# Performance work log

Hardware: AMD Instinct MI355X
Metric: run time of the kernel (lower is better)

## Reference

```python
import jax, jax.numpy as jnp
import numpy as np
import math

DIM, NH, HD = 4096, 32, 128
B, S = 2, 2048
MAX_SEQ, INIT_SLICE = 4096, 2048  # init_slice = max_seq_len - max_prompt_size
NEG = -1e9


def setup_inputs() -> dict:
    key = jax.random.key(0)
    ks = jax.random.split(key, 6)
    x = jax.random.normal(ks[0], (B, S, DIM), dtype=jnp.float32)
    scale = 1.0 / math.sqrt(DIM)
    wq = jax.random.normal(ks[1], (DIM, DIM), dtype=jnp.float32) * scale
    wk = jax.random.normal(ks[2], (DIM, DIM), dtype=jnp.float32) * scale
    wv = jax.random.normal(ks[3], (DIM, DIM), dtype=jnp.float32) * scale
    wo = jax.random.normal(ks[4], (DIM, DIM), dtype=jnp.float32) * scale
    # RoPE frequencies, viewed as real pairs [S, HD//2, 2] = (cos, sin)
    inv_freq = 1.0 / (10000.0 ** (jnp.arange(0, HD, 2, dtype=jnp.float32) / HD))
    ang = jnp.arange(S, dtype=jnp.float32)[:, None] * inv_freq[None, :]  # [S, HD//2]
    freqs_cis_real = jnp.stack([jnp.cos(ang), jnp.sin(ang)], axis=-1)
    # causal additive mask [1,1,S,S]
    mask = jnp.where(jnp.triu(jnp.ones((S, S), dtype=bool), k=1), NEG, 0.0)[None, None].astype(jnp.float32)
    cache_k = jnp.zeros((B, MAX_SEQ, NH, HD), dtype=jnp.float32)
    cache_v = jnp.zeros((B, MAX_SEQ, NH, HD), dtype=jnp.float32)
    return {"x": x, "freqs_cis_real": freqs_cis_real, "mask": mask,
            "wq": wq, "wk": wk, "wv": wv, "wo": wo,
            "cache_k": cache_k, "cache_v": cache_v, "slice_size": 2048}


def _apply_rotary(xq, xk, freqs_cis_real):
    # xq, xk: [b, s, h, d]; pairs along last dim are (real, imag)
    b, s, h, d = xq.shape
    fr = freqs_cis_real[None, :, None, :, 0]  # [1, s, 1, d//2]
    fi = freqs_cis_real[None, :, None, :, 1]

    def rot(t):
        t = t.reshape(b, s, h, d // 2, 2)
        tr, ti = t[..., 0], t[..., 1]
        out = jnp.stack([tr * fr - ti * fi, tr * fi + ti * fr], axis=-1)
        return out.reshape(b, s, h, d)

    return rot(xq), rot(xk)


def reference(x, freqs_cis_real, mask, wq, wk, wv, wo, cache_k, cache_v, slice_size):
    bsz, seqlen, _ = x.shape
    xq = (x @ wq.T).reshape(bsz, seqlen, NH, HD)
    xk = (x @ wk.T).reshape(bsz, seqlen, NH, HD)
    xv = (x @ wv.T).reshape(bsz, seqlen, NH, HD)
    xq, xk = _apply_rotary(xq, xk, freqs_cis_real)
    # prompt-phase (seqlen > 1) cache update: cat(cache[:, :init_slice], new)
    cache_k_new = jnp.concatenate([cache_k[:bsz, :INIT_SLICE], xk], axis=1)
    cache_v_new = jnp.concatenate([cache_v[:bsz, :INIT_SLICE], xv], axis=1)
    keys = cache_k_new[:, -slice_size:]    # [b, k, h, d]
    values = cache_v_new[:, -slice_size:]
    scores = jnp.einsum('bqhd,bkhd->bhqk', xq, keys) / math.sqrt(HD)
    scores = scores + mask
    probs = jax.nn.softmax(scores.astype(jnp.float32), axis=-1).astype(xq.dtype)
    out = jnp.einsum('bhqk,bkhd->bqhd', probs, values).reshape(bsz, seqlen, -1)
    return out @ wo.T
```

## Files before the change

### kernel.cpp

```cpp
#include <hip/hip_runtime.h>
#include <hip/hip_bf16.h>
#include <stdint.h>

#define SEQ   2048
#define NHEAD 32
#define HDIM  128
#define DMODEL 4096
#define MTOT  4096
#define RSCALE 0.08838834764831845f

typedef __hip_bfloat16 bf16_t;
typedef __attribute__((ext_vector_type(8))) short short8v;
typedef __attribute__((ext_vector_type(4))) short short4v;
typedef __attribute__((ext_vector_type(4))) float f32x4;

typedef __attribute__((address_space(3))) void lds_void;
typedef __attribute__((address_space(1))) void gbl_void;
#define TO_LDS(p) ((lds_void*)(uint32_t)(uintptr_t)(p))
#define TO_GBL(p) ((gbl_void*)(uintptr_t)(p))
#define ASYNC_CP16(g, l) __builtin_amdgcn_global_load_lds(TO_GBL(g), TO_LDS(l), 16, 0, 0)

__device__ __forceinline__ float bf2f(short u) {
  union { uint32_t i; float f; } x; x.i = ((uint32_t)(uint16_t)u) << 16; return x.f;
}

__global__ __launch_bounds__(256) void cast_f32_to_bf16(const float* __restrict__ in,
                                                        bf16_t* __restrict__ out) {
  size_t i = (size_t)blockIdx.x * 256 + threadIdx.x;
  const f32x4* p = (const f32x4*)in + i * 2;
  f32x4 a = p[0], b = p[1];
  __align__(16) bf16_t tmp[8];
#pragma unroll
  for (int j = 0; j < 4; ++j) tmp[j]     = __float2bfloat16(a[j]);
#pragma unroll
  for (int j = 0; j < 4; ++j) tmp[4 + j] = __float2bfloat16(b[j]);
  *(short8v*)(out + i * 8) = *(const short8v*)tmp;
}

#define GEMM_SUBITER(J, VMC, DO_ISSUE)                                         \
  {                                                                            \
    asm volatile("s_waitcnt vmcnt(" #VMC ")" ::: "memory");                    \
    __builtin_amdgcn_s_barrier();                                              \
    __builtin_amdgcn_sched_barrier(0);                                         \
    const char* sl = (const char*)&lds[(J) & 3][0];                            \
    short8v a[8], b[4];                                                        \
    _Pragma("unroll")                                                          \
    for (int m = 0; m < 8; ++m)                                                \
      a[m] = *(const short8v*)(sl + aoff + m * 1024);                          \
    _Pragma("unroll")                                                          \
    for (int n = 0; n < 4; ++n)                                                \
      b[n] = *(const short8v*)(sl + boff + n * 1024);                          \
    if (DO_ISSUE) {                                                            \
      const int jn = (J) + 3;                                                  \
      char* dl = (char*)&lds[jn & 3][0] + stoff;                               \
      const bf16_t* ga = gA + (size_t)jn * 32;                                 \
      const bf16_t* gb = gB + (size_t)jn * 32;                                 \
      ASYNC_CP16(ga,              dl);                                         \
      ASYNC_CP16(ga + 128 * 4096, dl + 8192);                                  \
      ASYNC_CP16(gb,              dl + 16384);                                 \
      ASYNC_CP16(gb + 128 * 4096, dl + 24576);                                 \
    }                                                                          \
    __builtin_amdgcn_s_setprio(1);                                             \
    _Pragma("unroll")                                                          \
    for (int m = 0; m < 8; ++m)                                                \
      _Pragma("unroll")                                                        \
      for (int n = 0; n < 4; ++n)                                              \
        acc[m][n] = __builtin_amdgcn_mfma_f32_16x16x32_bf16(a[m], b[n],        \
                                                            acc[m][n], 0, 0, 0); \
    __builtin_amdgcn_s_setprio(0);                                             \
  }

template <bool OUT_BF16>
__global__ __launch_bounds__(512, 2) void gemm_nt(const bf16_t* __restrict__ A,
                                                  const bf16_t* __restrict__ B0,
                                                  const bf16_t* __restrict__ B1,
                                                  const bf16_t* __restrict__ B2,
                                                  void* __restrict__ Cout) {
  __shared__ bf16_t lds[4][16384];
  const int z = blockIdx.z;
  const bf16_t* __restrict__ Bm = (z == 0) ? B0 : (z == 1 ? B1 : B2);
  const int tid = threadIdx.x;
  const int wave = tid >> 6, lane = tid & 63;
  const int bid = blockIdx.x;
  const int xcd = bid & 7, idx = bid >> 3;
  const int bm = (xcd >> 1) * 4 + (idx >> 3);
  const int bn = (xcd & 1) * 8 + (idx & 7);
  const int wr = wave >> 2, wc = wave & 3;
  const int r = lane & 15, g = lane >> 4;

  f32x4 acc[8][4] = {};

  const int srow = wave * 16 + (lane >> 2);
  const int scol = (lane & 3) * 8;
  const bf16_t* gA = A  + ((size_t)bm * 256 + srow) * 4096 + scol;
  const bf16_t* gB = Bm + ((size_t)bn * 256 + srow) * 4096 + scol;
  const int stoff = wave * 1024 + lane * 16;

  const int aoff = (wr * 128 + r) * 64 + g * 16;
  const int boff = 16384 + (wc * 64 + r) * 64 + g * 16;

#pragma unroll
  for (int j0 = 0; j0 < 3; ++j0) {
    char* dl = (char*)&lds[j0][0] + stoff;
    const bf16_t* ga = gA + (size_t)j0 * 32;
    const bf16_t* gb = gB + (size_t)j0 * 32;
    ASYNC_CP16(ga,              dl);
    ASYNC_CP16(ga + 128 * 4096, dl + 8192);
    ASYNC_CP16(gb,              dl + 16384);
    ASYNC_CP16(gb + 128 * 4096, dl + 24576);
  }

  for (int j = 0; j < 125; ++j) GEMM_SUBITER(j, 8, true);
  GEMM_SUBITER(125, 8, false);
  GEMM_SUBITER(126, 4, false);
  GEMM_SUBITER(127, 0, false);

  const size_t row_base = (size_t)bm * 256 + wr * 128 + g * 4;
  const size_t col_base = (size_t)bn * 256 + wc * 64 + r;
  if (OUT_BF16) {
    bf16_t* C = (bf16_t*)Cout + (size_t)z * 16777216u;
#pragma unroll
    for (int m = 0; m < 8; ++m)
#pragma unroll
      for (int n = 0; n < 4; ++n)
#pragma unroll
        for (int j = 0; j < 4; ++j)
          C[(row_base + m * 16 + j) * 4096 + col_base + n * 16] = __float2bfloat16(acc[m][n][j]);
  } else {
    float* C = (float*)Cout;
#pragma unroll
    for (int m = 0; m < 8; ++m)
#pragma unroll
      for (int n = 0; n < 4; ++n)
#pragma unroll
        for (int j = 0; j < 4; ++j)
          C[(row_base + m * 16 + j) * 4096 + col_base + n * 16] = acc[m][n][j];
  }
}

__global__ __launch_bounds__(256) void rope_kernel(const bf16_t* __restrict__ qkv,
                                                   const float* __restrict__ freqs,
                                                   bf16_t* __restrict__ qrot,
                                                   bf16_t* __restrict__ krot) {
  const int which = blockIdx.y;
  const bf16_t* __restrict__ src = qkv + (size_t)which * 16777216u;
  bf16_t* __restrict__ dst = (which == 0) ? qrot : krot;
  const float sc = (which == 0) ? RSCALE : 1.0f;
  size_t t = (size_t)blockIdx.x * 256 + threadIdx.x;
  int dg = t & 15;
  int s  = (int)(t >> 4) & 2047;
  int bh = (int)(t >> 15);
  int b  = bh >> 5;
  int d0 = dg * 8;

  short8v v = *(const short8v*)&src[((size_t)(b * 2048 + s)) * 4096 + (bh & 31) * 128 + d0];
  const float* fp = freqs + (size_t)s * 128 + d0;
  f32x4 f0 = *(const f32x4*)fp;
  f32x4 f1 = *(const f32x4*)(fp + 4);
  float fr[4] = {f0[0], f0[2], f1[0], f1[2]};
  float fi[4] = {f0[1], f0[3], f1[1], f1[3]};
  __align__(16) bf16_t tmp[8];
#pragma unroll
  for (int i = 0; i < 4; ++i) {
    float tr = bf2f(v[2 * i]), ti = bf2f(v[2 * i + 1]);
    tmp[2 * i]     = __float2bfloat16((tr * fr[i] - ti * fi[i]) * sc);
    tmp[2 * i + 1] = __float2bfloat16((tr * fi[i] + ti * fr[i]) * sc);
  }
  *(short8v*)&dst[((size_t)bh * 2048 + s) * 128 + d0] = *(const short8v*)tmp;
}

__global__ __launch_bounds__(256) void vtrans_kernel(const bf16_t* __restrict__ xv,
                                                     bf16_t* __restrict__ vt) {
  __shared__ bf16_t tile[64 * 136];
  const int s0 = blockIdx.x * 64;
  const int bh = blockIdx.y;
  const int b = bh >> 5, h = bh & 31;
  const int tid = threadIdx.x;
#pragma unroll
  for (int it = 0; it < 4; ++it) {
    int c = it * 256 + tid;
    int row = c >> 4, col8 = c & 15;
    short8v v = *(const short8v*)&xv[((size_t)(b * 2048 + s0 + row)) * 4096 + h * 128 + col8 * 8];
    *(short8v*)&tile[row * 136 + col8 * 8] = v;
  }
  __syncthreads();
#pragma unroll
  for (int it = 0; it < 4; ++it) {
    int c = it * 256 + tid;
    int d = c >> 3, sc = c & 7;
    __align__(16) bf16_t tmp[8];
#pragma unroll
    for (int i = 0; i < 8; ++i) tmp[i] = tile[(sc * 8 + i) * 136 + d];
    *(short8v*)&vt[((size_t)(bh * 128 + d)) * 2048 + s0 + sc * 8] = *(const short8v*)tmp;
  }
}

#define PSTR 72
__global__ __launch_bounds__(512) void attn_kernel(const bf16_t* __restrict__ qrot,
                                                   const bf16_t* __restrict__ krot,
                                                   const bf16_t* __restrict__ vt,
                                                   bf16_t* __restrict__ att) {
  __shared__ bf16_t Kls[64 * 128];
  __shared__ bf16_t Vls[128 * 64];
  __shared__ bf16_t Pls[8][16 * PSTR];

  const int lid  = blockIdx.x;
  const int xcd  = lid & 7;
  const int kk_  = lid >> 3;
  const int bh   = xcd + 8 * ((kk_ >> 4) & 7);
  const int qidx = 15 - (kk_ & 15);
  const int warp = threadIdx.x >> 6;
  const int lane = threadIdx.x & 63;
  const int r = lane & 15, g = lane >> 4;

  const bf16_t* __restrict__ Q  = qrot + (size_t)bh * 2048 * 128;
  const bf16_t* __restrict__ Kp = krot + (size_t)bh * 2048 * 128;
  const bf16_t* __restrict__ Vt = vt   + (size_t)bh * 128 * 2048;
  bf16_t* __restrict__ Pw = &Pls[warp][0];

  const int qB = qidx * 128 + warp * 16;
  const int ntiles = 2 * qidx + 2;

  short8v qf[4];
#pragma unroll
  for (int kk = 0; kk < 4; ++kk)
    qf[kk] = *(const short8v*)&Q[(size_t)(qB + r) * 128 + kk * 32 + g * 8];

  float l = 0.f;
  f32x4 o[8];
#pragma unroll
  for (int n2 = 0; n2 < 8; ++n2) o[n2] = f32x4{0.f, 0.f, 0.f, 0.f};

  const int rA = lane >> 4, cA = lane & 15;
  const int rB = lane >> 3, cB = lane & 7;
  const int swz = (r & 7) << 4;

  for (int t = 0; t < ntiles; ++t) {
    const int kb = t * 64;

#pragma unroll
    for (int i = 0; i < 2; ++i) {
      const int krow = warp * 8 + i * 4 + rA;
      const int kcol = 8 * (cA ^ ((i * 4 + rA) & 7));
      ASYNC_CP16(Kp + (size_t)(kb + krow) * 128 + kcol,
                 (char*)Kls + (size_t)(krow * 128 + cA * 8) * 2);
    }
#pragma unroll
    for (int i = 0; i < 2; ++i) {
      const int vrow = warp * 16 + i * 8 + rB;
      const int vcol = 8 * (cB ^ rB);
      ASYNC_CP16(Vt + (size_t)vrow * 2048 + kb + vcol,
                 (char*)Vls + (size_t)(vrow * 64 + cB * 8) * 2);
    }
    __syncthreads();

    if (kb <= qB + 15) {
      f32x4 sacc[4];
#pragma unroll
      for (int n = 0; n < 4; ++n) sacc[n] = f32x4{0.f, 0.f, 0.f, 0.f};
#pragma unroll
      for (int n = 0; n < 4; ++n)
#pragma unroll
        for (int kk = 0; kk < 4; ++kk) {
          short8v kf = *(const short8v*)((const char*)Kls +
                         (n * 16 + r) * 256 + ((kk * 64 + g * 16) ^ swz));
          sacc[n] = __builtin_amdgcn_mfma_f32_16x16x32_bf16(kf, qf[kk], sacc[n], 0, 0, 0);
        }

      float p[16];
#pragma unroll
      for (int n = 0; n < 4; ++n)
#pragma unroll
        for (int j = 0; j < 4; ++j)
          p[n * 4 + j] = __expf(sacc[n][j]);

      if (kb + 63 > qB) {
        const int qa = qB + r;
#pragma unroll
        for (int n = 0; n < 4; ++n)
#pragma unroll
          for (int j = 0; j < 4; ++j)
            if (kb + n * 16 + g * 4 + j > qa) p[n * 4 + j] = 0.f;
      }

      {
        float ts[8];
#pragma unroll
        for (int i = 0; i < 8; ++i) ts[i] = p[i] + p[i + 8];
#pragma unroll
        for (int i = 0; i < 4; ++i) ts[i] += ts[i + 4];
        float rs = (ts[0] + ts[1]) + (ts[2] + ts[3]);
        rs += __shfl_xor(rs, 16, 64);
        rs += __shfl_xor(rs, 32, 64);
        l += rs;
      }

#pragma unroll
      for (int n = 0; n < 4; ++n) {
        __align__(8) bf16_t tp[4];
#pragma unroll
        for (int j = 0; j < 4; ++j) tp[j] = __float2bfloat16(p[n * 4 + j]);
        *(short4v*)&Pw[r * PSTR + n * 16 + g * 4] = *(const short4v*)tp;
      }

#pragma unroll
      for (int kk2 = 0; kk2 < 2; ++kk2) {
        short8v pf = *(const short8v*)&Pw[r * PSTR + kk2 * 32 + g * 8];
#pragma unroll
        for (int n2 = 0; n2 < 8; ++n2) {
          short8v vf = *(const short8v*)((const char*)Vls +
                         (n2 * 16 + r) * 128 + ((kk2 * 64 + g * 16) ^ swz));
          o[n2] = __builtin_amdgcn_mfma_f32_16x16x32_bf16(pf, vf, o[n2], 0, 0, 0);
        }
      }
    }
    __syncthreads();
  }

  float lq[4];
#pragma unroll
  for (int j = 0; j < 4; ++j) lq[j] = 1.0f / __shfl(l, g * 4 + j, 64);
  const int b = bh >> 5, h = bh & 31;
#pragma unroll
  for (int n2 = 0; n2 < 8; ++n2)
#pragma unroll
    for (int j = 0; j < 4; ++j)
      att[((size_t)(b * 2048 + qB + g * 4 + j)) * 4096 + h * 128 + n2 * 16 + r] =
          __float2bfloat16(o[n2][j] * lq[j]);
}

extern "C" void kernel_launch(void* const* d_in, const int* in_sizes, int n_in,
                              void* d_out, int out_size, void* d_ws, size_t ws_size,
                              hipStream_t stream) {
  (void)in_sizes; (void)n_in; (void)out_size; (void)ws_size;
  const float* x  = (const float*)d_in[0];
  const float* fr = (const float*)d_in[1];
  const float* wq = (const float*)d_in[3];
  const float* wk = (const float*)d_in[4];
  const float* wv = (const float*)d_in[5];
  const float* wo = (const float*)d_in[6];

  char* ws = (char*)d_ws;
  const size_t MB32 = 33554432;
  bf16_t* xb  = (bf16_t*)(ws + 0 * MB32);
  bf16_t* wqb = (bf16_t*)(ws + 1 * MB32);
  bf16_t* wkb = (bf16_t*)(ws + 2 * MB32);
  bf16_t* wvb = (bf16_t*)(ws + 3 * MB32);
  bf16_t* qkv = (bf16_t*)(ws + 4 * MB32);

  cast_f32_to_bf16<<<8192, 256, 0, stream>>>(x,  xb);
  cast_f32_to_bf16<<<8192, 256, 0, stream>>>(wq, wqb);
  cast_f32_to_bf16<<<8192, 256, 0, stream>>>(wk, wkb);
  cast_f32_to_bf16<<<8192, 256, 0, stream>>>(wv, wvb);

  gemm_nt<true><<<dim3(256, 1, 3), 512, 0, stream>>>(xb, wqb, wkb, wvb, (void*)qkv);

  bf16_t* qrot = xb;
  bf16_t* krot = wqb;
  bf16_t* vtp  = wkb;
  bf16_t* attb = wvb;

  rope_kernel<<<dim3(8192, 2), 256, 0, stream>>>(qkv, fr, qrot, krot);
  vtrans_kernel<<<dim3(32, 64), 256, 0, stream>>>(qkv + 2 * 16777216u, vtp);

  bf16_t* wob = qkv;
  cast_f32_to_bf16<<<8192, 256, 0, stream>>>(wo, wob);

  attn_kernel<<<1024, 512, 0, stream>>>(qrot, krot, vtp, attb);

  gemm_nt<false><<<dim3(256, 1, 1), 512, 0, stream>>>(attb, wob, wob, wob, d_out);
}
```

Measured before the change: 713.7 us.

## Restructure GEMM mainloop into 64-wide K tiles with swizzled LDS and quadrant-staged prefetch

Replaces the 4-stage, 32-wide K pipeline in the NT GEMM with a double-buffered 64-wide K tile that uses an XOR-swizzled LDS layout. Each tile is split into four MFMA quadrants, and the loads for the next tile are issued in pieces between them. Block-to-tile mapping is also changed so each XCD owns two full row stripes. The aim is fewer barriers per K step, fewer LDS bank conflicts, better L2 locality, and global loads overlapping compute. The trade-off is that wait counts and barriers are now hand-tuned and fragile, and there is less prefetch depth, so load latency may be exposed.

```diff
diff --git a/kernel.cpp b/kernel.cpp
--- a/kernel.cpp
+++ b/kernel.cpp
@@ -37,36 +37,90 @@
   *(short8v*)(out + i * 8) = *(const short8v*)tmp;
 }
 
-#define GEMM_SUBITER(J, VMC, DO_ISSUE)                                         \
+#define VMW_(N) asm volatile("s_waitcnt vmcnt(" #N ")" ::: "memory")
+#define VMW(N) VMW_(N)
+
+#define STAGE_A(mh_, X)                                                        \
+  { const int tr_ = tid >> 3, c_ = tid & 7;                                    \
+    _Pragma("unroll")                                                          \
+    for (int i_ = 0; i_ < 2; ++i_) {                                           \
+      const int row_ = (mh_) * 64 + i_ * 128 + tr_;                            \
+      const int cg_ = c_ ^ (row_ & 7);                                         \
+      ASYNC_CP16(gA0 + (size_t)row_ * 4096 + (size_t)(X) * 64 + cg_ * 8,       \
+                 ldsc + (((X) & 1) << 16) + row_ * 128 + c_ * 16); } }
+
+#define STAGE_B(nh_, X)                                                        \
+  { const int tr_ = tid >> 3, c_ = tid & 7;                                    \
+    _Pragma("unroll")                                                          \
+    for (int i_ = 0; i_ < 2; ++i_) {                                           \
+      const int row_ = i_ * 128 + (tr_ >> 5) * 64 + (nh_) * 32 + (tr_ & 31);   \
+      const int cg_ = c_ ^ (row_ & 7);                                         \
+      ASYNC_CP16(gB0 + (size_t)row_ * 4096 + (size_t)(X) * 64 + cg_ * 8,       \
+                 ldsc + (((X) & 1) << 16) + 32768 + row_ * 128 + c_ * 16); } }
+
+#define TILE4(T, DOSTG, VA, VB, VC)                                            \
   {                                                                            \
-    asm volatile("s_waitcnt vmcnt(" #VMC ")" ::: "memory");                    \
+    const int sb = ((T) & 1) << 16;                                            \
+    const int Xn = (T) + 1;                                                    \
+    short8v a0[4][2], a1[4][2], b0[2][2], b1[2][2];                            \
+                                                 \
+    VMW(VA);                                                                   \
     __builtin_amdgcn_s_barrier();                                              \
     __builtin_amdgcn_sched_barrier(0);                                         \
-    const char* sl = (const char*)&lds[(J) & 3][0];                            \
-    short8v a[8], b[4];                                                        \
-    _Pragma("unroll")                                                          \
-    for (int m = 0; m < 8; ++m)                                                \
-      a[m] = *(const short8v*)(sl + aoff + m * 1024);                          \
-    _Pragma("unroll")                                                          \
-    for (int n = 0; n < 4; ++n)                                                \
-      b[n] = *(const short8v*)(sl + boff + n * 1024);                          \
-    if (DO_ISSUE) {                                                            \
-      const int jn = (J) + 3;                                                  \
-      char* dl = (char*)&lds[jn & 3][0] + stoff;                               \
-      const bf16_t* ga = gA + (size_t)jn * 32;                                 \
-      const bf16_t* gb = gB + (size_t)jn * 32;                                 \
-      ASYNC_CP16(ga,              dl);                                         \
-      ASYNC_CP16(ga + 128 * 4096, dl + 8192);                                  \
-      ASYNC_CP16(gb,              dl + 16384);                                 \
-      ASYNC_CP16(gb + 128 * 4096, dl + 24576);                                 \
-    }                                                                          \
+    _Pragma("unroll") for (int m = 0; m < 4; ++m)                              \
+      _Pragma("unroll") for (int kk = 0; kk < 2; ++kk)                         \
+        a0[m][kk] = *(const short8v*)(ldsc + sb + aRow + m * 2048 + (kk ? cx1 : cx0)); \
+    _Pragma("unroll") for (int n = 0; n < 2; ++n)                              \
+      _Pragma("unroll") for (int kk = 0; kk < 2; ++kk)                         \
+        b0[n][kk] = *(const short8v*)(ldsc + sb + bRow + n * 2048 + (kk ? cx1 : cx0)); \
+    if (DOSTG) STAGE_A(0, Xn);                                                 \
+    asm volatile("s_waitcnt lgkmcnt(0)" ::: "memory");                         \
+    __builtin_amdgcn_sched_barrier(0);                                         \
     __builtin_amdgcn_s_setprio(1);                                             \
-    _Pragma("unroll")                                                          \
-    for (int m = 0; m < 8; ++m)                                                \
-      _Pragma("unroll")                                                        \
-      for (int n = 0; n < 4; ++n)                                              \
-        acc[m][n] = __builtin_amdgcn_mfma_f32_16x16x32_bf16(a[m], b[n],        \
-                                                            acc[m][n], 0, 0, 0); \
+    _Pragma("unroll") for (int m = 0; m < 4; ++m)                              \
+      _Pragma("unroll") for (int n = 0; n < 2; ++n)                            \
+        _Pragma("unroll") for (int kk = 0; kk < 2; ++kk)                       \
+          acc[m][n] = __builtin_amdgcn_mfma_f32_16x16x32_bf16(a0[m][kk], b0[n][kk], acc[m][n], 0, 0, 0); \
+    __builtin_amdgcn_s_setprio(0);                                             \
+                                                 \
+    VMW(VB);                                                                   \
+    __builtin_amdgcn_s_barrier();                                              \
+    __builtin_amdgcn_sched_barrier(0);                                         \
+    _Pragma("unroll") for (int n = 0; n < 2; ++n)                              \
+      _Pragma("unroll") for (int kk = 0; kk < 2; ++kk)                         \
+        b1[n][kk] = *(const short8v*)(ldsc + sb + bRow + 4096 + n * 2048 + (kk ? cx1 : cx0)); \
+    if (DOSTG) STAGE_B(0, Xn);                                                 \
+    asm volatile("s_waitcnt lgkmcnt(0)" ::: "memory");                         \
+    __builtin_amdgcn_sched_barrier(0);                                         \
+    __builtin_amdgcn_s_setprio(1);                                             \
+    _Pragma("unroll") for (int m = 0; m < 4; ++m)                              \
+      _Pragma("unroll") for (int n = 0; n < 2; ++n)                            \
+        _Pragma("unroll") for (int kk = 0; kk < 2; ++kk)                       \
+          acc[m][2 + n] = __builtin_amdgcn_mfma_f32_16x16x32_bf16(a0[m][kk], b1[n][kk], acc[m][2 + n], 0, 0, 0); \
+    __builtin_amdgcn_s_setprio(0);                                             \
+                                                 \
+    VMW(VC);                                                                   \
+    __builtin_amdgcn_s_barrier();                                              \
+    __builtin_amdgcn_sched_barrier(0);                                         \
+    _Pragma("unroll") for (int m = 0; m < 4; ++m)                              \
+      _Pragma("unroll") for (int kk = 0; kk < 2; ++kk)                         \
+        a1[m][kk] = *(const short8v*)(ldsc + sb + aRow + 8192 + m * 2048 + (kk ? cx1 : cx0)); \
+    if (DOSTG) STAGE_B(1, Xn);                                                 \
+    asm volatile("s_waitcnt lgkmcnt(0)" ::: "memory");                         \
+    __builtin_amdgcn_sched_barrier(0);                                         \
+    __builtin_amdgcn_s_setprio(1);                                             \
+    _Pragma("unroll") for (int m = 0; m < 4; ++m)                              \
+      _Pragma("unroll") for (int n = 0; n < 2; ++n)                            \
+        _Pragma("unroll") for (int kk = 0; kk < 2; ++kk)                       \
+          acc[4 + m][2 + n] = __builtin_amdgcn_mfma_f32_16x16x32_bf16(a1[m][kk], b1[n][kk], acc[4 + m][2 + n], 0, 0, 0); \
+    __builtin_amdgcn_s_setprio(0);                                             \
+     \
+    if (DOSTG) STAGE_A(1, Xn);                                                 \
+    __builtin_amdgcn_s_setprio(1);                                             \
+    _Pragma("unroll") for (int m = 0; m < 4; ++m)                              \
+      _Pragma("unroll") for (int n = 0; n < 2; ++n)                            \
+        _Pragma("unroll") for (int kk = 0; kk < 2; ++kk)                       \
+          acc[4 + m][n] = __builtin_amdgcn_mfma_f32_16x16x32_bf16(a1[m][kk], b0[n][kk], acc[4 + m][n], 0, 0, 0); \
     __builtin_amdgcn_s_setprio(0);                                             \
   }
 
@@ -76,44 +130,37 @@
                                                   const bf16_t* __restrict__ B1,
                                                   const bf16_t* __restrict__ B2,
                                                   void* __restrict__ Cout) {
-  __shared__ bf16_t lds[4][16384];
+  __shared__ __align__(16) char ldsbuf[131072];
+  char* ldsc = ldsbuf;
   const int z = blockIdx.z;
   const bf16_t* __restrict__ Bm = (z == 0) ? B0 : (z == 1 ? B1 : B2);
   const int tid = threadIdx.x;
   const int wave = tid >> 6, lane = tid & 63;
   const int bid = blockIdx.x;
   const int xcd = bid & 7, idx = bid >> 3;
-  const int bm = (xcd >> 1) * 4 + (idx >> 3);
-  const int bn = (xcd & 1) * 8 + (idx & 7);
+  const int bm = xcd * 2 + (idx >> 4);
+  const int bn = idx & 15;
   const int wr = wave >> 2, wc = wave & 3;
   const int r = lane & 15, g = lane >> 4;
 
   f32x4 acc[8][4] = {};
 
-  const int srow = wave * 16 + (lane >> 2);
-  const int scol = (lane & 3) * 8;
-  const bf16_t* gA = A  + ((size_t)bm * 256 + srow) * 4096 + scol;
-  const bf16_t* gB = Bm + ((size_t)bn * 256 + srow) * 4096 + scol;
-  const int stoff = wave * 1024 + lane * 16;
-
-  const int aoff = (wr * 128 + r) * 64 + g * 16;
-  const int boff = 16384 + (wc * 64 + r) * 64 + g * 16;
-
-#pragma unroll
-  for (int j0 = 0; j0 < 3; ++j0) {
-    char* dl = (char*)&lds[j0][0] + stoff;
-    const bf16_t* ga = gA + (size_t)j0 * 32;
-    const bf16_t* gb = gB + (size_t)j0 * 32;
-    ASYNC_CP16(ga,              dl);
-    ASYNC_CP16(ga + 128 * 4096, dl + 8192);
-    ASYNC_CP16(gb,              dl + 16384);
-    ASYNC_CP16(gb + 128 * 4096, dl + 24576);
-  }
-
-  for (int j = 0; j < 125; ++j) GEMM_SUBITER(j, 8, true);
-  GEMM_SUBITER(125, 8, false);
-  GEMM_SUBITER(126, 4, false);
-  GEMM_SUBITER(127, 0, false);
+  const bf16_t* gA0 = A  + (size_t)bm * 256 * 4096;
+  const bf16_t* gB0 = Bm + (size_t)bn * 256 * 4096;
+
+  const int swz = r & 7;
+  const int cx0 = (g ^ swz) << 4;
+  const int cx1 = ((4 + g) ^ swz) << 4;
+  const int aRow = (wr * 128 + r) * 128;
+  const int bRow = 32768 + (wc * 64 + r) * 128;
+
+  STAGE_A(0, 0);
+  STAGE_B(0, 0);
+  STAGE_B(1, 0);
+  STAGE_A(1, 0);
+
+  for (int T = 0; T < 63; ++T) TILE4(T, 1, 4, 4, 4);
+  TILE4(63, 0, 4, 2, 0);
 
   const size_t row_base = (size_t)bm * 256 + wr * 128 + g * 4;
   const size_t col_base = (size_t)bn * 256 + wc * 64 + r;
```

Result: faster. 666.6 us (-6.6%).
